# Kernel optimization log

Hardware: AMD Instinct MI355X
Metric: run time of the kernel (lower is better)

Reference implementation:

```python
import jax, jax.numpy as jnp
import numpy as np

N_NODES = 100000
N_EDGES = 50000
NNZ = 1000000


def _scatter_mean(vals, idx, num_segments):
    s = jax.ops.segment_sum(vals, idx, num_segments=num_segments)
    cnt = jax.ops.segment_sum(jnp.ones((vals.shape[0],), vals.dtype), idx, num_segments=num_segments)
    return s / jnp.maximum(cnt, 1.0)[:, None]


def _normalize_l2(X):
    # row L2 normalize; scale computed on detached values, inf -> 0
    norm = jnp.linalg.norm(X, axis=1, keepdims=True)
    scale = jax.lax.stop_gradient(jnp.where(norm > 0, 1.0 / norm, 0.0))
    return X * scale


def _conv(X, W, V, E, homo, use_norm):
    # X: [N, in], W: [in, heads*out]
    X = X @ W                                   # [N, D]
    Xve = X[V]                                  # gather vertex -> incidence [nnz, D]
    Xe = _scatter_mean(Xve, E, N_EDGES)         # first_aggregate='mean' -> [nE, D]
    Xev = Xe[E]                                 # gather edge -> incidence [nnz, D]
    he = homo[E]                                # [nnz]
    att_sum = jax.ops.segment_sum(he, V, num_segments=N_NODES)[V]  # [nnz]
    att = (he / att_sum)[:, None]               # [nnz, 1]
    Xv = jax.ops.segment_sum(att * Xev, V, num_segments=N_NODES)   # second_aggregate='sum' -> [N, D]
    X = X + Xv
    if use_norm:
        X = _normalize_l2(X)
    return X


def setup_inputs() -> dict:
    key = jax.random.key(0)
    k1, k2, k3, k4, k5, k6, k7 = jax.random.split(key, 7)
    nfeat, dh, nclass = 256, 256, 40  # dh = nhid*nhead = 64*4
    X = jax.random.normal(k1, (N_NODES, nfeat), dtype=jnp.float32)
    V = jax.random.randint(k2, (NNZ,), 0, N_NODES)
    E = jax.random.randint(k3, (NNZ,), 0, N_EDGES)
    homo = jax.random.uniform(k4, (N_EDGES,), dtype=jnp.float32, minval=0.1, maxval=1.0)
    s1 = 1.0 / np.sqrt(nfeat)
    s2 = 1.0 / np.sqrt(dh)
    W1 = jax.random.uniform(k5, (nfeat, dh), dtype=jnp.float32, minval=-s1, maxval=s1)
    W2 = jax.random.uniform(k6, (dh, dh), dtype=jnp.float32, minval=-s2, maxval=s2)
    Wout = jax.random.uniform(k7, (dh, nclass), dtype=jnp.float32, minval=-s2, maxval=s2)
    return {"X": X, "V": V, "E": E, "homo": homo, "W1": W1, "W2": W2, "Wout": Wout}


def reference(X, V, E, homo, W1, W2, Wout):
    # HHyperGNN.forward (eval mode: dropouts are identity), nlayer=3
    X = _conv(X, W1, V, E, homo, use_norm=True)
    X = jax.nn.relu(X)
    X = _conv(X, W2, V, E, homo, use_norm=True)
    X = jax.nn.relu(X)
    Z = X
    X = _conv(X, Wout, V, E, homo, use_norm=True)
    return (Z, X)
```

## Files before the change

### kernel.cpp

```cpp
#include <hip/hip_runtime.h>

#define NND 100000
#define NED 50000
#define NNZC 1000000
#define MGRID 1564
#define CNTB 512

typedef __attribute__((ext_vector_type(8))) short bf16x8;
typedef __attribute__((ext_vector_type(4))) float f32x4;

__device__ __forceinline__ float b2f(unsigned short u) {
  union { unsigned int u; float f; } x; x.u = ((unsigned int)u) << 16; return x.f;
}
__device__ __forceinline__ float blo(unsigned int u) {
  union { unsigned int u; float f; } x; x.u = u << 16; return x.f;
}
__device__ __forceinline__ float bhi(unsigned int u) {
  union { unsigned int u; float f; } x; x.u = u & 0xffff0000u; return x.f;
}
__device__ __forceinline__ unsigned short f2b(float f) {
  union { float f; unsigned int u; } x; x.f = f;
  unsigned int r = x.u + 0x7FFFu + ((x.u >> 16) & 1u);
  return (unsigned short)(r >> 16);
}
__device__ __forceinline__ unsigned int pk2(float lo, float hi) {
  return (unsigned int)f2b(lo) | ((unsigned int)f2b(hi) << 16);
}

__global__ void prep_f32(const void* __restrict__ Hin, const void* __restrict__ W1,
                         const void* __restrict__ W2, const void* __restrict__ Wout,
                         float* __restrict__ Hf, unsigned short* __restrict__ WT1b,
                         unsigned short* __restrict__ WT2b, float* __restrict__ Wf3,
                         int* __restrict__ mode) {
  __shared__ int ok;
  if (threadIdx.x == 0) ok = 1;
  __syncthreads();
  if (threadIdx.x < 64) {
    float v = b2f(((const unsigned short*)Hin)[threadIdx.x]);
    if (!(v >= 0.04f && v <= 1.1f)) ok = 0;
  }
  __syncthreads();
  int m = ok ? 0 : 1;
  int i = blockIdx.x * 256 + threadIdx.x;
  if (i == 0) *mode = m;
  if (i < 65536) {
    int n = i >> 8, k = i & 255;
    float w1 = m ? ((const float*)W1)[k * 256 + n] : b2f(((const unsigned short*)W1)[k * 256 + n]);
    float w2 = m ? ((const float*)W2)[k * 256 + n] : b2f(((const unsigned short*)W2)[k * 256 + n]);
    WT1b[i] = f2b(w1);
    WT2b[i] = f2b(w2);
  }
  if (i < 16384) {
    int k = i >> 6, n = i & 63;
    Wf3[i] = (n < 40)
      ? (m ? ((const float*)Wout)[k * 40 + n] : b2f(((const unsigned short*)Wout)[k * 40 + n]))
      : 0.f;
  }
  if (i < NED)
    Hf[i] = m ? ((const float*)Hin)[i] : b2f(((const unsigned short*)Hin)[i]);
}

__device__ __forceinline__ void gemm_body(
    const void* __restrict__ A, bool a_fp32,
    const unsigned short* __restrict__ WT,
    unsigned short* __restrict__ Cb, int M, int bid) {
  __shared__ unsigned short As[128][40];
  __shared__ unsigned short Bs[128][40];
  const int t = threadIdx.x;
  const int l = t & 63;
  const int w = t >> 6;
  const int wr = w >> 1, wc = w & 1;
  const int lr16 = l & 15, lg = l >> 4;
  const int bm = bid >> 1;
  const int n0 = (bid & 1) * 128;
  const int row0 = bm * 128;

  const int tr = t >> 1, th = t & 1;
  int arow = row0 + tr; if (arow >= M) arow = M - 1;

  f32x4 acc[4][4];
#pragma unroll
  for (int m = 0; m < 4; m++)
#pragma unroll
    for (int n = 0; n < 4; n++) acc[m][n] = (f32x4){0.f, 0.f, 0.f, 0.f};

  uint4 a0, a1, b0, b1;
  auto load_regs = [&](int k0) {
    if (a_fp32) {
      const float4* ap = (const float4*)((const float*)A + (size_t)arow * 256 + k0 + th * 16);
      float4 f0 = ap[0], f1 = ap[1], f2 = ap[2], f3 = ap[3];
      a0 = make_uint4(pk2(f0.x, f0.y), pk2(f0.z, f0.w), pk2(f1.x, f1.y), pk2(f1.z, f1.w));
      a1 = make_uint4(pk2(f2.x, f2.y), pk2(f2.z, f2.w), pk2(f3.x, f3.y), pk2(f3.z, f3.w));
    } else {
      const uint4* ap = (const uint4*)((const unsigned short*)A + (size_t)arow * 256 + k0 + th * 16);
      a0 = ap[0]; a1 = ap[1];
    }
    const uint4* bp = (const uint4*)(WT + (size_t)(n0 + tr) * 256 + k0 + th * 16);
    b0 = bp[0]; b1 = bp[1];
  };

  load_regs(0);
  for (int k0 = 0; k0 < 256; k0 += 32) {
    __syncthreads();
    *(uint4*)&As[tr][th * 16]     = a0;
    *(uint4*)&As[tr][th * 16 + 8] = a1;
    *(uint4*)&Bs[tr][th * 16]     = b0;
    *(uint4*)&Bs[tr][th * 16 + 8] = b1;
    __syncthreads();
    if (k0 < 224) load_regs(k0 + 32);

    bf16x8 af[4], bfr[4];
#pragma unroll
    for (int m = 0; m < 4; m++)
      af[m] = *(const bf16x8*)&As[wr * 64 + m * 16 + lr16][lg * 8];
#pragma unroll
    for (int n = 0; n < 4; n++)
      bfr[n] = *(const bf16x8*)&Bs[wc * 64 + n * 16 + lr16][lg * 8];
#pragma unroll
    for (int m = 0; m < 4; m++)
#pragma unroll
      for (int n = 0; n < 4; n++)
        acc[m][n] = __builtin_amdgcn_mfma_f32_16x16x32_bf16(af[m], bfr[n], acc[m][n], 0, 0, 0);
  }

#pragma unroll
  for (int m = 0; m < 4; m++) {
#pragma unroll
    for (int j = 0; j < 4; j++) {
      int row = row0 + wr * 64 + m * 16 + lg * 4 + j;
      if (row < M) {
#pragma unroll
        for (int n = 0; n < 4; n++)
          Cb[(size_t)row * 256 + n0 + wc * 64 + n * 16 + lr16] = f2b(acc[m][n][j]);
      }
    }
  }
}

__global__ __launch_bounds__(256) void gemm1_cnt(
    const void* __restrict__ A, const int* __restrict__ mode,
    const unsigned short* __restrict__ WT, unsigned short* __restrict__ Cb, int M,
    const int* __restrict__ V, const int* __restrict__ E,
    int* __restrict__ cntAll, unsigned short* __restrict__ rV,
    unsigned short* __restrict__ rE) {
  const int b = blockIdx.x;
  if (b < CNTB) {
    const int STRIDE = CNTB * 256;
    int i0 = b * 256 + threadIdx.x;
#pragma unroll
    for (int q = 0; q < 8; q++) {
      int i = i0 + q * STRIDE;
      if (i < NNZC) {
        unsigned short rv = (unsigned short)atomicAdd(&cntAll[V[i]], 1);
        unsigned short re = (unsigned short)atomicAdd(&cntAll[NND + E[i]], 1);
        rV[i] = rv;
        rE[i] = re;
      }
    }
    return;
  }
  gemm_body(A, *mode == 1, WT, Cb, M, b - CNTB);
}

__global__ __launch_bounds__(256) void gemm_bf16_k(
    const unsigned short* __restrict__ A, const unsigned short* __restrict__ WT,
    unsigned short* __restrict__ Cb, int M) {
  gemm_body(A, false, WT, Cb, M, blockIdx.x);
}

__global__ void scan_local(const int* __restrict__ in, int* __restrict__ outExcl,
                           int* __restrict__ bsum, int n) {
  __shared__ int s[256];
  int t = threadIdx.x;
  int i = blockIdx.x * 256 + t;
  int v = (i < n) ? in[i] : 0;
  s[t] = v;
  __syncthreads();
  for (int off = 1; off < 256; off <<= 1) {
    int x = (t >= off) ? s[t - off] : 0;
    __syncthreads();
    s[t] += x;
    __syncthreads();
  }
  if (i < n) outExcl[i] = s[t] - v;
  if (t == 255) bsum[blockIdx.x] = s[255];
}

__global__ void scan_add2(int* __restrict__ outExcl, const int* __restrict__ bsum,
                          int n) {
  __shared__ int sm[256];
  int b = blockIdx.x, t = threadIdx.x;
  int partial = 0;
  for (int j = t; j < b; j += 256) partial += bsum[j];
  sm[t] = partial;
  __syncthreads();
  for (int off = 128; off; off >>= 1) {
    if (t < off) sm[t] += sm[t + off];
    __syncthreads();
  }
  int total = sm[0];
  int i = b * 256 + t;
  if (i < n) outExcl[i] += total;
}

__global__ void fill_nr(const int* __restrict__ V, const int* __restrict__ E,
                        const int* __restrict__ offAll,
                        const unsigned short* __restrict__ rV,
                        const unsigned short* __restrict__ rE,
                        const float* __restrict__ Hf,
                        unsigned int* __restrict__ vadjH,
                        int* __restrict__ eadj) {
  int i = blockIdx.x * 256 + threadIdx.x;
  if (i < NNZC) {
    int v = V[i], e = E[i];
    vadjH[offAll[v] + rV[i]] = (unsigned int)e | ((unsigned int)f2b(Hf[e]) << 16);
    eadj[offAll[NND + e] - NNZC + rE[i]] = v;
  }
}

__global__ __launch_bounds__(256) void edge_gather_b(
    const int* __restrict__ eoff, const int* __restrict__ cntE,
    const int* __restrict__ eadj, const unsigned int* __restrict__ XWb,
    unsigned int* __restrict__ Xeb) {
  int e = blockIdx.x * 4 + (threadIdx.x >> 6);
  int tl = threadIdx.x & 63;
  if (e >= NED) return;
  int start = eoff[e] - NNZC, n = cntE[e];
  float a0 = 0.f, a1 = 0.f, a2 = 0.f, a3 = 0.f;
  for (int c0 = 0; c0 < n; c0 += 64) {
    int m = n - c0; if (m > 64) m = 64;
    int vidx = (tl < m) ? eadj[start + c0 + tl] : 0;
#pragma unroll 4
    for (int j = 0; j < m; j++) {
      int vv = __shfl(vidx, j);
      uint2 x = *((const uint2*)(XWb + (size_t)vv * 128) + tl);
      a0 += blo(x.x); a1 += bhi(x.x); a2 += blo(x.y); a3 += bhi(x.y);
    }
  }
  float inv = (n > 0) ? 1.0f / (float)n : 0.f;
  uint2 o;
  o.x = pk2(a0 * inv, a1 * inv);
  o.y = pk2(a2 * inv, a3 * inv);
  *((uint2*)(Xeb + (size_t)e * 128) + tl) = o;
}

__global__ __launch_bounds__(256) void node_gather_norm_b(
    const int* __restrict__ voff, const int* __restrict__ degV,
    const unsigned int* __restrict__ vadjH,
    const unsigned int* __restrict__ Xeb, const unsigned int* __restrict__ XWb,
    unsigned int* __restrict__ Zb, float* __restrict__ outf,
    const float* __restrict__ W3, unsigned short* __restrict__ XW64) {
  __shared__ float zrow[4][256];
  int wid = threadIdx.x >> 6;
  int v = blockIdx.x * 4 + wid;
  int tl = threadIdx.x & 63;
  int start = voff[v], n = degV[v];
  uint2 r = *((const uint2*)(XWb + (size_t)v * 128) + tl);
  float a0 = blo(r.x), a1 = bhi(r.x), a2 = blo(r.y), a3 = bhi(r.y);
  float g0 = 0.f, g1 = 0.f, g2 = 0.f, g3 = 0.f, hsum = 0.f;
  for (int c0 = 0; c0 < n; c0 += 64) {
    int m = n - c0; if (m > 64) m = 64;
    unsigned int pk = (tl < m) ? vadjH[start + c0 + tl] : 0u;
    hsum += b2f((unsigned short)(pk >> 16));
#pragma unroll 4
    for (int j = 0; j < m; j++) {
      unsigned int u = (unsigned int)__shfl((int)pk, j);
      int ee = (int)(u & 0xffffu);
      float a = b2f((unsigned short)(u >> 16));
      uint2 x = *((const uint2*)(Xeb + (size_t)ee * 128) + tl);
      g0 += a * blo(x.x); g1 += a * bhi(x.x);
      g2 += a * blo(x.y); g3 += a * bhi(x.y);
    }
  }
#pragma unroll
  for (int off = 32; off; off >>= 1) hsum += __shfl_xor(hsum, off);
  float inv_att = (hsum > 0.f) ? 1.0f / hsum : 0.f;
  a0 += inv_att * g0; a1 += inv_att * g1;
  a2 += inv_att * g2; a3 += inv_att * g3;
  float ss = a0 * a0 + a1 * a1 + a2 * a2 + a3 * a3;
#pragma unroll
  for (int off = 32; off; off >>= 1) ss += __shfl_xor(ss, off);
  float sc = (ss > 0.f) ? (1.0f / sqrtf(ss)) : 0.f;
  a0 = fmaxf(a0 * sc, 0.f); a1 = fmaxf(a1 * sc, 0.f);
  a2 = fmaxf(a2 * sc, 0.f); a3 = fmaxf(a3 * sc, 0.f);
  if (Zb) {
    uint2 o; o.x = pk2(a0, a1); o.y = pk2(a2, a3);
    *((uint2*)(Zb + (size_t)v * 128) + tl) = o;
  }
  if (outf) *((float4*)(outf + (size_t)v * 256) + tl) = make_float4(a0, a1, a2, a3);
  if (W3) {
    *(float4*)&zrow[wid][tl * 4] = make_float4(a0, a1, a2, a3);
    __syncthreads();
    float out = 0.f;
#pragma unroll 4
    for (int k = 0; k < 256; k += 4) {
      float4 z4 = *(const float4*)&zrow[wid][k];
      out += z4.x * W3[(k + 0) * 64 + tl];
      out += z4.y * W3[(k + 1) * 64 + tl];
      out += z4.z * W3[(k + 2) * 64 + tl];
      out += z4.w * W3[(k + 3) * 64 + tl];
    }
    XW64[(size_t)v * 64 + tl] = f2b(out);
  }
}

__global__ __launch_bounds__(256) void edge_gather_64(
    const int* __restrict__ eoff, const int* __restrict__ cntE,
    const int* __restrict__ eadj, const unsigned short* __restrict__ XW64,
    unsigned short* __restrict__ Xe64) {
  int e = blockIdx.x * 4 + (threadIdx.x >> 6);
  int tl = threadIdx.x & 63;
  if (e >= NED) return;
  int start = eoff[e] - NNZC, n = cntE[e];
  float ax = 0.f;
  for (int c0 = 0; c0 < n; c0 += 64) {
    int m = n - c0; if (m > 64) m = 64;
    int vidx = (tl < m) ? eadj[start + c0 + tl] : 0;
#pragma unroll 4
    for (int j = 0; j < m; j++) {
      int vv = __shfl(vidx, j);
      ax += b2f(XW64[(size_t)vv * 64 + tl]);
    }
  }
  float inv = (n > 0) ? 1.0f / (float)n : 0.f;
  Xe64[(size_t)e * 64 + tl] = f2b(ax * inv);
}

__global__ __launch_bounds__(256) void node_gather_norm_64(
    const int* __restrict__ voff, const int* __restrict__ degV,
    const unsigned int* __restrict__ vadjH,
    const unsigned short* __restrict__ Xe64, const unsigned short* __restrict__ XW64,
    float* __restrict__ out) {
  int v = blockIdx.x * 4 + (threadIdx.x >> 6);
  int tl = threadIdx.x & 63;
  if (v >= NND) return;
  int start = voff[v], n = degV[v];
  float ax = b2f(XW64[(size_t)v * 64 + tl]);
  float gx = 0.f, hsum = 0.f;
  for (int c0 = 0; c0 < n; c0 += 64) {
    int m = n - c0; if (m > 64) m = 64;
    unsigned int pk = (tl < m) ? vadjH[start + c0 + tl] : 0u;
    hsum += b2f((unsigned short)(pk >> 16));
#pragma unroll 4
    for (int j = 0; j < m; j++) {
      unsigned int u = (unsigned int)__shfl((int)pk, j);
      int ee = (int)(u & 0xffffu);
      float a = b2f((unsigned short)(u >> 16));
      gx += a * b2f(Xe64[(size_t)ee * 64 + tl]);
    }
  }
#pragma unroll
  for (int off = 32; off; off >>= 1) hsum += __shfl_xor(hsum, off);
  float inv_att = (hsum > 0.f) ? 1.0f / hsum : 0.f;
  ax += inv_att * gx;
  float ss = ax * ax;
#pragma unroll
  for (int off = 32; off; off >>= 1) ss += __shfl_xor(ss, off);
  float sc = (ss > 0.f) ? (1.0f / sqrtf(ss)) : 0.f;
  ax *= sc;
  if (tl < 40) out[(size_t)v * 40 + tl] = ax;
}

__global__ void sentinel_k(float* __restrict__ out, long n, float val) {
  long i = (long)blockIdx.x * 256 + threadIdx.x;
  long stride = (long)gridDim.x * 256;
  for (; i < n; i += stride) out[i] = val;
}

extern "C" void kernel_launch(void* const* d_in, const int* in_sizes, int n_in,
                              void* d_out, int out_size, void* d_ws, size_t ws_size,
                              hipStream_t stream) {
  const void* Xin  = d_in[0];
  const int*  V    = (const int*)d_in[1];
  const int*  E    = (const int*)d_in[2];
  const void* Hin  = d_in[3];
  const void* W1   = d_in[4];
  const void* W2   = d_in[5];
  const void* Wout = d_in[6];
  float* Zout = (float*)d_out;
  float* Xout = Zout + (size_t)NND * 256;
  (void)in_sizes; (void)n_in;

  char* base = (char*)d_ws;
  size_t o = 0;
  auto carve = [&](size_t bytes) -> char* {
    char* p = base + o;
    o += (bytes + 255) & ~(size_t)255;
    return p;
  };
  unsigned int*  XWb  = (unsigned int*)carve((size_t)NND * 256 * 2);
  unsigned int*  Xeb  = (unsigned int*)carve((size_t)NED * 256 * 2);
  unsigned int*  Zb   = (unsigned int*)carve((size_t)NND * 256 * 2);
  unsigned short* XW64 = (unsigned short*)carve((size_t)NND * 64 * 2);
  unsigned short* Xe64 = (unsigned short*)carve((size_t)NED * 64 * 2);
  float* Hf    = (float*)carve((size_t)NED * 4);
  int*   cntAll = (int*)carve((size_t)(NND + NED) * 4);
  int*   offAll = (int*)carve((size_t)(NND + NED) * 4);
  unsigned short* rV = (unsigned short*)carve((size_t)NNZC * 2);
  unsigned short* rE = (unsigned short*)carve((size_t)NNZC * 2);
  unsigned int* vadjH = (unsigned int*)carve((size_t)NNZC * 4);
  int*   eadj  = (int*)carve((size_t)NNZC * 4);
  int*   bsum  = (int*)carve(1024 * 4);
  unsigned short* WT1b = (unsigned short*)carve(65536 * 2);
  unsigned short* WT2b = (unsigned short*)carve(65536 * 2);
  float* Wf3   = (float*)carve(16384 * 4);
  int*   mode  = (int*)carve(256);
  const size_t NEED = o;

  if (ws_size < NEED) {
    sentinel_k<<<4096, 256, 0, stream>>>(Zout, (long)out_size, 77.0f);
    return;
  }

  const int NCNT = NND + NED;
  const int NBC = (NCNT + 255) / 256;
  const int FILL_GRID = (NNZC + 255) / 256;
  const int EG_GRID = (NED + 3) / 4;
  const int NG_GRID = (NND + 3) / 4;

  const int* voff = offAll;
  const int* eoff = offAll + NND;
  const int* degV = cntAll;
  const int* cntE = cntAll + NND;

  prep_f32<<<256, 256, 0, stream>>>(Hin, W1, W2, Wout, Hf, WT1b, WT2b, Wf3, mode);
  hipMemsetAsync(cntAll, 0, (size_t)NCNT * 4, stream);

  gemm1_cnt<<<CNTB + MGRID, 256, 0, stream>>>(Xin, mode, WT1b, (unsigned short*)XWb,
                                              NND, V, E, cntAll, rV, rE);

  scan_local<<<NBC, 256, 0, stream>>>(cntAll, offAll, bsum, NCNT);
  scan_add2<<<NBC, 256, 0, stream>>>(offAll, bsum, NCNT);
  fill_nr<<<FILL_GRID, 256, 0, stream>>>(V, E, offAll, rV, rE, Hf, vadjH, eadj);

  edge_gather_b<<<EG_GRID, 256, 0, stream>>>(eoff, cntE, eadj, XWb, Xeb);
  node_gather_norm_b<<<NG_GRID, 256, 0, stream>>>(voff, degV, vadjH, Xeb, XWb,
                                                  Zb, nullptr, nullptr, nullptr);

  gemm_bf16_k<<<MGRID, 256, 0, stream>>>((const unsigned short*)Zb, WT2b,
                                         (unsigned short*)XWb, NND);
  edge_gather_b<<<EG_GRID, 256, 0, stream>>>(eoff, cntE, eadj, XWb, Xeb);
  node_gather_norm_b<<<NG_GRID, 256, 0, stream>>>(voff, degV, vadjH, Xeb, XWb,
                                                  nullptr, Zout, Wf3, XW64);

  edge_gather_64<<<EG_GRID, 256, 0, stream>>>(eoff, cntE, eadj, XW64, Xe64);
  node_gather_norm_64<<<NG_GRID, 256, 0, stream>>>(voff, degV, vadjH, Xe64, XW64, Xout);
}
```

Baseline: 967.1 us.

## Move layer-3 projection to MFMA GEMM and overlap vadj fill with edge gather

```diff
diff --git a/kernel.cpp b/kernel.cpp
--- a/kernel.cpp
+++ b/kernel.cpp
@@ -5,6 +5,7 @@
 #define NNZC 1000000
 #define MGRID 1564
 #define CNTB 512
+#define FILLB 512
 
 typedef __attribute__((ext_vector_type(8))) short bf16x8;
 typedef __attribute__((ext_vector_type(4))) float f32x4;
@@ -30,7 +31,8 @@
 __global__ void prep_f32(const void* __restrict__ Hin, const void* __restrict__ W1,
                          const void* __restrict__ W2, const void* __restrict__ Wout,
                          float* __restrict__ Hf, unsigned short* __restrict__ WT1b,
-                         unsigned short* __restrict__ WT2b, float* __restrict__ Wf3,
+                         unsigned short* __restrict__ WT2b,
+                         unsigned short* __restrict__ WT3b,
                          int* __restrict__ mode) {
   __shared__ int ok;
   if (threadIdx.x == 0) ok = 1;
@@ -51,10 +53,11 @@
     WT2b[i] = f2b(w2);
   }
   if (i < 16384) {
-    int k = i >> 6, n = i & 63;
-    Wf3[i] = (n < 40)
+    int n = i >> 8, k = i & 255;
+    float w3 = (n < 40)
       ? (m ? ((const float*)Wout)[k * 40 + n] : b2f(((const unsigned short*)Wout)[k * 40 + n]))
       : 0.f;
+    WT3b[i] = f2b(w3);
   }
   if (i < NED)
     Hf[i] = m ? ((const float*)Hin)[i] : b2f(((const unsigned short*)Hin)[i]);
@@ -168,6 +171,72 @@
   gemm_body(A, false, WT, Cb, M, blockIdx.x);
 }
 
+__global__ __launch_bounds__(256) void gemm3_mfma(
+    const unsigned short* __restrict__ A, const unsigned short* __restrict__ WT,
+    unsigned short* __restrict__ Cb, int M) {
+  __shared__ unsigned short As[128][40];
+  __shared__ unsigned short Bs[64][40];
+  const int t = threadIdx.x;
+  const int l = t & 63;
+  const int w = t >> 6;
+  const int wr = w >> 1, wc = w & 1;
+  const int lr16 = l & 15, lg = l >> 4;
+  const int row0 = blockIdx.x * 128;
+
+  const int tr = t >> 1, th = t & 1;
+  const int br = t >> 2, bq = t & 3;
+  int arow = row0 + tr; if (arow >= M) arow = M - 1;
+
+  f32x4 acc[4][2];
+#pragma unroll
+  for (int m = 0; m < 4; m++)
+#pragma unroll
+    for (int n = 0; n < 2; n++) acc[m][n] = (f32x4){0.f, 0.f, 0.f, 0.f};
+
+  uint4 a0, a1, b0;
+  auto load_regs = [&](int k0) {
+    const uint4* ap = (const uint4*)(A + (size_t)arow * 256 + k0 + th * 16);
+    a0 = ap[0]; a1 = ap[1];
+    b0 = *(const uint4*)(WT + (size_t)br * 256 + k0 + bq * 8);
+  };
+
+  load_regs(0);
+  for (int k0 = 0; k0 < 256; k0 += 32) {
+    __syncthreads();
+    *(uint4*)&As[tr][th * 16]     = a0;
+    *(uint4*)&As[tr][th * 16 + 8] = a1;
+    *(uint4*)&Bs[br][bq * 8]      = b0;
+    __syncthreads();
+    if (k0 < 224) load_regs(k0 + 32);
+
+    bf16x8 af[4], bfr[2];
+#pragma unroll
+    for (int m = 0; m < 4; m++)
+      af[m] = *(const bf16x8*)&As[wr * 64 + m * 16 + lr16][lg * 8];
+#pragma unroll
+    for (int n = 0; n < 2; n++)
+      bfr[n] = *(const bf16x8*)&Bs[wc * 32 + n * 16 + lr16][lg * 8];
+#pragma unroll
+    for (int m = 0; m < 4; m++)
+#pragma unroll
+      for (int n = 0; n < 2; n++)
+        acc[m][n] = __builtin_amdgcn_mfma_f32_16x16x32_bf16(af[m], bfr[n], acc[m][n], 0, 0, 0);
+  }
+
+#pragma unroll
+  for (int m = 0; m < 4; m++) {
+#pragma unroll
+    for (int j = 0; j < 4; j++) {
+      int row = row0 + wr * 64 + m * 16 + lg * 4 + j;
+      if (row < M) {
+#pragma unroll
+        for (int n = 0; n < 2; n++)
+          Cb[(size_t)row * 64 + wc * 32 + n * 16 + lr16] = f2b(acc[m][n][j]);
+      }
+    }
+  }
+}
+
 __global__ void scan_local(const int* __restrict__ in, int* __restrict__ outExcl,
                            int* __restrict__ bsum, int n) {
   __shared__ int s[256];
@@ -203,26 +272,33 @@
   if (i < n) outExcl[i] += total;
 }
 
-__global__ void fill_nr(const int* __restrict__ V, const int* __restrict__ E,
-                        const int* __restrict__ offAll,
-                        const unsigned short* __restrict__ rV,
-                        const unsigned short* __restrict__ rE,
-                        const float* __restrict__ Hf,
-                        unsigned int* __restrict__ vadjH,
-                        int* __restrict__ eadj) {
+__global__ void fill_e(const int* __restrict__ V, const int* __restrict__ E,
+                       const int* __restrict__ offAll,
+                       const unsigned short* __restrict__ rE,
+                       int* __restrict__ eadj) {
   int i = blockIdx.x * 256 + threadIdx.x;
   if (i < NNZC) {
-    int v = V[i], e = E[i];
-    vadjH[offAll[v] + rV[i]] = (unsigned int)e | ((unsigned int)f2b(Hf[e]) << 16);
-    eadj[offAll[NND + e] - NNZC + rE[i]] = v;
+    int e = E[i];
+    eadj[offAll[NND + e] - NNZC + rE[i]] = V[i];
   }
 }
 
 __global__ __launch_bounds__(256) void edge_gather_b(
     const int* __restrict__ eoff, const int* __restrict__ cntE,
     const int* __restrict__ eadj, const unsigned int* __restrict__ XWb,
-    unsigned int* __restrict__ Xeb) {
-  int e = blockIdx.x * 4 + (threadIdx.x >> 6);
+    unsigned int* __restrict__ Xeb, int fillv,
+    const int* __restrict__ V, const int* __restrict__ E,
+    const int* __restrict__ offAll, const unsigned short* __restrict__ rV,
+    const float* __restrict__ Hf, unsigned int* __restrict__ vadjH) {
+  if (blockIdx.x < fillv) {
+    const int stride = fillv * 256;
+    for (int i = blockIdx.x * 256 + threadIdx.x; i < NNZC; i += stride) {
+      int v = V[i], e = E[i];
+      vadjH[offAll[v] + rV[i]] = (unsigned int)e | ((unsigned int)f2b(Hf[e]) << 16);
+    }
+    return;
+  }
+  int e = (blockIdx.x - fillv) * 4 + (threadIdx.x >> 6);
   int tl = threadIdx.x & 63;
   if (e >= NED) return;
   int start = eoff[e] - NNZC, n = cntE[e];
@@ -248,12 +324,10 @@
     const int* __restrict__ voff, const int* __restrict__ degV,
     const unsigned int* __restrict__ vadjH,
     const unsigned int* __restrict__ Xeb, const unsigned int* __restrict__ XWb,
-    unsigned int* __restrict__ Zb, float* __restrict__ outf,
-    const float* __restrict__ W3, unsigned short* __restrict__ XW64) {
-  __shared__ float zrow[4][256];
-  int wid = threadIdx.x >> 6;
-  int v = blockIdx.x * 4 + wid;
+    unsigned int* __restrict__ Zb, float* __restrict__ outf) {
+  int v = blockIdx.x * 4 + (threadIdx.x >> 6);
   int tl = threadIdx.x & 63;
+  if (v >= NND) return;
   int start = voff[v], n = degV[v];
   uint2 r = *((const uint2*)(XWb + (size_t)v * 128) + tl);
   float a0 = blo(r.x), a1 = bhi(r.x), a2 = blo(r.y), a3 = bhi(r.y);
@@ -288,20 +362,6 @@
     *((uint2*)(Zb + (size_t)v * 128) + tl) = o;
   }
   if (outf) *((float4*)(outf + (size_t)v * 256) + tl) = make_float4(a0, a1, a2, a3);
-  if (W3) {
-    *(float4*)&zrow[wid][tl * 4] = make_float4(a0, a1, a2, a3);
-    __syncthreads();
-    float out = 0.f;
-#pragma unroll 4
-    for (int k = 0; k < 256; k += 4) {
-      float4 z4 = *(const float4*)&zrow[wid][k];
-      out += z4.x * W3[(k + 0) * 64 + tl];
-      out += z4.y * W3[(k + 1) * 64 + tl];
-      out += z4.z * W3[(k + 2) * 64 + tl];
-      out += z4.w * W3[(k + 3) * 64 + tl];
-    }
-    XW64[(size_t)v * 64 + tl] = f2b(out);
-  }
 }
 
 __global__ __launch_bounds__(256) void edge_gather_64(
@@ -403,7 +463,7 @@
   int*   bsum  = (int*)carve(1024 * 4);
   unsigned short* WT1b = (unsigned short*)carve(65536 * 2);
   unsigned short* WT2b = (unsigned short*)carve(65536 * 2);
-  float* Wf3   = (float*)carve(16384 * 4);
+  unsigned short* WT3b = (unsigned short*)carve(16384 * 2);
   int*   mode  = (int*)carve(256);
   const size_t NEED = o;
 
@@ -417,13 +477,14 @@
   const int FILL_GRID = (NNZC + 255) / 256;
   const int EG_GRID = (NED + 3) / 4;
   const int NG_GRID = (NND + 3) / 4;
+  const int G3_GRID = (NND + 127) / 128;
 
   const int* voff = offAll;
   const int* eoff = offAll + NND;
   const int* degV = cntAll;
   const int* cntE = cntAll + NND;
 
-  prep_f32<<<256, 256, 0, stream>>>(Hin, W1, W2, Wout, Hf, WT1b, WT2b, Wf3, mode);
+  prep_f32<<<256, 256, 0, stream>>>(Hin, W1, W2, Wout, Hf, WT1b, WT2b, WT3b, mode);
   hipMemsetAsync(cntAll, 0, (size_t)NCNT * 4, stream);
 
   gemm1_cnt<<<CNTB + MGRID, 256, 0, stream>>>(Xin, mode, WT1b, (unsigned short*)XWb,
@@ -431,18 +492,21 @@
 
   scan_local<<<NBC, 256, 0, stream>>>(cntAll, offAll, bsum, NCNT);
   scan_add2<<<NBC, 256, 0, stream>>>(offAll, bsum, NCNT);
-  fill_nr<<<FILL_GRID, 256, 0, stream>>>(V, E, offAll, rV, rE, Hf, vadjH, eadj);
-
-  edge_gather_b<<<EG_GRID, 256, 0, stream>>>(eoff, cntE, eadj, XWb, Xeb);
+  fill_e<<<FILL_GRID, 256, 0, stream>>>(V, E, offAll, rE, eadj);
+
+  edge_gather_b<<<FILLB + EG_GRID, 256, 0, stream>>>(
+      eoff, cntE, eadj, XWb, Xeb, FILLB, V, E, offAll, rV, Hf, vadjH);
   node_gather_norm_b<<<NG_GRID, 256, 0, stream>>>(voff, degV, vadjH, Xeb, XWb,
-                                                  Zb, nullptr, nullptr, nullptr);
+                                                  Zb, nullptr);
 
   gemm_bf16_k<<<MGRID, 256, 0, stream>>>((const unsigned short*)Zb, WT2b,
                                          (unsigned short*)XWb, NND);
-  edge_gather_b<<<EG_GRID, 256, 0, stream>>>(eoff, cntE, eadj, XWb, Xeb);
+  edge_gather_b<<<EG_GRID, 256, 0, stream>>>(
+      eoff, cntE, eadj, XWb, Xeb, 0, nullptr, nullptr, nullptr, nullptr, nullptr, nullptr);
   node_gather_norm_b<<<NG_GRID, 256, 0, stream>>>(voff, degV, vadjH, Xeb, XWb,
-                                                  nullptr, Zout, Wf3, XW64);
-
+                                                  Zb, Zout);
+
+  gemm3_mfma<<<G3_GRID, 256, 0, stream>>>((const unsigned short*)Zb, WT3b, XW64, NND);
   edge_gather_64<<<EG_GRID, 256, 0, stream>>>(eoff, cntE, eadj, XW64, Xe64);
   node_gather_norm_64<<<NG_GRID, 256, 0, stream>>>(voff, degV, vadjH, Xe64, XW64, Xout);
 }
```

New measurement: 853.6 us. -11.7%, faster.
